# Kernel tuning notes

Measured on AMD Instinct MI355X. Metric: run time of the kernel, lower is better.

The kernel has to match this reference:

```python
import jax, jax.numpy as jnp
import numpy as np

B, S, D, H = 2, 2048, 1024, 16
HEAD_DIM = D // H  # 64


def setup_inputs() -> dict:
    key = jax.random.key(0)
    ks = jax.random.split(key, 7)
    x = jax.random.normal(ks[0], (B, S, D), dtype=jnp.float32)
    W_q = jax.random.normal(ks[1], (D, D), dtype=jnp.float32) * 0.02
    W_k = jax.random.normal(ks[2], (D, D), dtype=jnp.float32) * 0.02
    W_v = jax.random.normal(ks[3], (D, D), dtype=jnp.float32) * 0.02
    W_o = jax.random.normal(ks[4], (D, D), dtype=jnp.float32) * 0.02 / np.sqrt(2 * 12)
    b_o = jnp.zeros((D,), dtype=jnp.float32)
    # Ragged prefix attention_mask: per-row valid lengths in [S/2, S];
    # row 0 forced to full length so max_valid_len == S statically (jit-safe).
    lengths = jax.random.randint(ks[5], (B,), S // 2, S + 1)
    lengths = lengths.at[0].set(S)
    attention_mask = (jnp.arange(S)[None, :] < lengths[:, None]).astype(jnp.float32)
    return {"x": x, "attention_mask": attention_mask, "W_q": W_q, "W_k": W_k,
            "W_v": W_v, "W_o": W_o, "b_o": b_o}


def reference(x, attention_mask, W_q, W_k, W_v, W_o, b_o):
    b, s, d = x.shape
    h, hd = H, HEAD_DIM
    # QKV projections (no bias, qkv_bias=False)
    q = (x @ W_q.T).reshape(b, s, h, hd).transpose(0, 2, 1, 3)  # [b,h,s,hd]
    # Masking keys/values at invalid (padded) positions; for prefix masks this
    # is exactly the module's per-batch packing loop (max_valid_len == s).
    m = attention_mask[:, None, :, None]  # [b,1,s,1]
    k = ((x @ W_k.T).reshape(b, s, h, hd).transpose(0, 2, 1, 3)) * m
    v = ((x @ W_v.T).reshape(b, s, h, hd).transpose(0, 2, 1, 3)) * m
    # Naive causal attention, same op order as the torch module:
    # mask with -inf first, then scale by 1/sqrt(head_dim), then softmax.
    causal = jnp.triu(jnp.ones((s, s), dtype=bool), 1)  # True above diagonal
    scores = jnp.einsum('bhqd,bhkd->bhqk', q, k)
    scores = jnp.where(causal[None, None], -jnp.inf, scores)
    att = jax.nn.softmax(scores / jnp.sqrt(jnp.float32(hd)), axis=-1)
    ctx = jnp.einsum('bhqk,bhkd->bhqd', att, v)  # [b,h,s,hd]
    ctx = ctx.transpose(0, 2, 1, 3).reshape(b, s, d)
    # Output projection (dropout is inference no-op)
    return ctx @ W_o.T + b_o
```

## Files before the change

kernel.cpp:

```cpp
#include <hip/hip_runtime.h>

#define B_  2
#define S_  2048
#define D_  1024
#define H_  16
#define HD_ 64
#define N3_ 3072
#define M_  4096

typedef _Float16 f16;
typedef _Float16 f16x2 __attribute__((ext_vector_type(2)));
typedef _Float16 f16x4 __attribute__((ext_vector_type(4)));
typedef _Float16 f16x8 __attribute__((ext_vector_type(8)));
typedef float    f32x4 __attribute__((ext_vector_type(4)));

__device__ __forceinline__ void async16(const f16* g, f16* l) {
  __builtin_amdgcn_global_load_lds(
      (const __attribute__((address_space(1))) unsigned int*)g,
      (__attribute__((address_space(3))) unsigned int*)l, 16, 0, 0);
}

__device__ __forceinline__ f16x2 pkrtz(float a, float b) {
  return __builtin_bit_cast(f16x2, __builtin_amdgcn_cvt_pkrtz(a, b));
}

__device__ __forceinline__ float vexp2(float x) {
  float r; asm("v_exp_f32 %0, %1" : "=v"(r) : "v"(x)); return r;
}

__global__ __launch_bounds__(256)
void cvt_all(const float* __restrict__ x,
             const float* __restrict__ Wq, const float* __restrict__ Wk,
             const float* __restrict__ Wv, const float* __restrict__ Wo,
             f16* __restrict__ xb, f16* __restrict__ wdst, float qscale) {
  const int i = blockIdx.x * 256 + threadIdx.x;
  const int XN4 = M_ * D_ / 4;
  const int WN4 = D_ * D_ / 4;
  const float* src;
  f16* dst;
  float scale = 1.0f;
  int j;
  if (i < XN4) {
    src = x; dst = xb; j = i;
  } else {
    int k = i - XN4;
    int m = k >> 18;
    j = k & (WN4 - 1);
    src = (m == 0) ? Wq : (m == 1) ? Wk : (m == 2) ? Wv : Wo;
    if (m == 0) scale = qscale;
    dst = wdst + (size_t)m * D_ * D_;
  }
  float4 v = ((const float4*)src)[j];
  f16x4 o = { (f16)(v.x * scale), (f16)(v.y * scale),
              (f16)(v.z * scale), (f16)(v.w * scale) };
  ((f16x4*)dst)[j] = o;
}

__global__ __launch_bounds__(256)
void gemm_qkv(const f16* __restrict__ A, const f16* __restrict__ Bw,
              f16* __restrict__ Cq, f16* __restrict__ vtout,
              const float* __restrict__ mask) {
  __shared__ f16 As0[64 * 64];
  __shared__ f16 Bs0[128 * 64];
  __shared__ f16 As1[64 * 64];
  __shared__ f16 Bs1[128 * 64];

  const int tid  = threadIdx.x;
  const int lane = tid & 63;
  const int w    = tid >> 6;
  const int lcol = lane & 15;
  const int quad = lane >> 4;
  const int lx   = lcol & 7;
  const int wave_m = w >> 1, wave_n = w & 1;

  const int lin  = blockIdx.x;
  const int xcd  = lin & 7;
  const int c    = lin >> 3;
  const int mIdx = c / 12;
  const int nIdx = c - mIdx * 12;
  const int m0 = ((xcd >> 1) * 16 + mIdx) * 64;
  const int n0 = ((xcd & 1) * 12 + nIdx) * 128;

  const int rr  = lane >> 3;
  const int gch = (lane & 7) ^ rr;

  const f16* gA[2];
  const f16* gB[4];
#pragma unroll
  for (int i = 0; i < 2; i++) {
    int seg = 2 * w + i;
    gA[i] = A + (size_t)(m0 + seg * 8 + rr) * D_ + gch * 8;
  }
#pragma unroll
  for (int i = 0; i < 4; i++) {
    int seg = i * 4 + w;
    gB[i] = Bw + (size_t)(n0 + seg * 8 + rr) * D_ + gch * 8;
  }

  int offA[2], offB[4];
#pragma unroll
  for (int i = 0; i < 2; i++) offA[i] = (wave_m * 32 + i * 16 + lcol) * 64;
#pragma unroll
  for (int i = 0; i < 4; i++) offB[i] = (wave_n * 64 + i * 16 + lcol) * 64;

  const f32x4 zero = {0.f, 0.f, 0.f, 0.f};
  f32x4 acc[2][4];
#pragma unroll
  for (int i = 0; i < 2; i++)
#pragma unroll
    for (int j = 0; j < 4; j++) acc[i][j] = zero;

  auto stage = [&](int k0, f16* sA, f16* sB) {
#pragma unroll
    for (int i = 0; i < 2; i++) async16(gA[i] + k0, sA + (2 * w + i) * 512);
#pragma unroll
    for (int i = 0; i < 4; i++) async16(gB[i] + k0, sB + (i * 4 + w) * 512);
  };
  auto compute = [&](const f16* sA, const f16* sB) {
#pragma unroll
    for (int ks = 0; ks < 2; ks++) {
      const int co = ((quad + 4 * ks) ^ lx) * 8;
      f16x8 af[2], bf[4];
#pragma unroll
      for (int i = 0; i < 2; i++) af[i] = *(const f16x8*)(sA + offA[i] + co);
#pragma unroll
      for (int i = 0; i < 4; i++) bf[i] = *(const f16x8*)(sB + offB[i] + co);
#pragma unroll
      for (int mi = 0; mi < 2; mi++)
#pragma unroll
        for (int ni = 0; ni < 4; ni++)
          acc[mi][ni] = __builtin_amdgcn_mfma_f32_16x16x32_f16(
              af[mi], bf[ni], acc[mi][ni], 0, 0, 0);
    }
  };

  stage(0, As0, Bs0);
  for (int it = 0; it < 14; it += 2) {
    stage((it + 1) * 64, As1, Bs1);
    asm volatile("s_waitcnt vmcnt(6)\ns_barrier" ::: "memory");
    compute(As0, Bs0);
    asm volatile("s_barrier" ::: "memory");
    stage((it + 2) * 64, As0, Bs0);
    asm volatile("s_waitcnt vmcnt(6)\ns_barrier" ::: "memory");
    compute(As1, Bs1);
    asm volatile("s_barrier" ::: "memory");
  }
  stage(15 * 64, As1, Bs1);
  asm volatile("s_waitcnt vmcnt(6)\ns_barrier" ::: "memory");
  compute(As0, Bs0);
  asm volatile("s_waitcnt vmcnt(0)\ns_barrier" ::: "memory");
  compute(As1, Bs1);

#pragma unroll
  for (int mi = 0; mi < 2; mi++) {
    const int mgb = m0 + wave_m * 32 + mi * 16 + quad * 4;
    const int bb = mgb >> 11, s = mgb & (S_ - 1);
    const float mk0 = mask[mgb], mk1 = mask[mgb + 1];
    const float mk2 = mask[mgb + 2], mk3 = mask[mgb + 3];
    const float mks[4] = {mk0, mk1, mk2, mk3};
    if (n0 >= 2 * D_) {
#pragma unroll
      for (int ni = 0; ni < 4; ni++) {
        const int vcol = n0 - 2 * D_ + wave_n * 64 + ni * 16 + lcol;
        f16x4 v = { (f16)(acc[mi][ni][0] * mk0), (f16)(acc[mi][ni][1] * mk1),
                    (f16)(acc[mi][ni][2] * mk2), (f16)(acc[mi][ni][3] * mk3) };
        *(f16x4*)(vtout +
                  ((size_t)(bb * 16 + (vcol >> 6)) * 64 + (vcol & 63)) * S_ + s) = v;
      }
    } else {
      const bool kmask = (n0 >= D_);
#pragma unroll
      for (int r = 0; r < 4; r++) {
        const float mk = kmask ? mks[r] : 1.0f;
#pragma unroll
        for (int ni = 0; ni < 4; ni++) {
          int ng = n0 + wave_n * 64 + ni * 16 + lcol;
          Cq[(size_t)(mgb + r) * N3_ + ng] = (f16)(acc[mi][ni][r] * mk);
        }
      }
    }
  }
}

__global__ __launch_bounds__(256)
void gemm_proj(const f16* __restrict__ A, const f16* __restrict__ Bw,
               float* __restrict__ Cf, const float* __restrict__ bias) {
  __shared__ f16 As[64 * 64];
  __shared__ f16 Bs[128 * 64];

  const int tid  = threadIdx.x;
  const int lane = tid & 63;
  const int w    = tid >> 6;
  const int lcol = lane & 15;
  const int quad = lane >> 4;
  const int lx   = lcol & 7;
  const int wave_m = w >> 1, wave_n = w & 1;

  const int m0 = blockIdx.y * 64;
  const int n0 = blockIdx.x * 128;

  const int rr  = lane >> 3;
  const int gch = (lane & 7) ^ rr;

  const f16* gA[2];
  const f16* gB[4];
  f16* lA[2];
  f16* lB[4];
#pragma unroll
  for (int i = 0; i < 2; i++) {
    int seg = 2 * w + i;
    gA[i] = A + (size_t)(m0 + seg * 8 + rr) * D_ + gch * 8;
    lA[i] = As + seg * 512;
  }
#pragma unroll
  for (int i = 0; i < 4; i++) {
    int seg = i * 4 + w;
    gB[i] = Bw + (size_t)(n0 + seg * 8 + rr) * D_ + gch * 8;
    lB[i] = Bs + seg * 512;
  }

  int offA[2], offB[4];
#pragma unroll
  for (int i = 0; i < 2; i++) offA[i] = (wave_m * 32 + i * 16 + lcol) * 64;
#pragma unroll
  for (int i = 0; i < 4; i++) offB[i] = (wave_n * 64 + i * 16 + lcol) * 64;

  const f32x4 zero = {0.f, 0.f, 0.f, 0.f};
  f32x4 acc[2][4];
#pragma unroll
  for (int i = 0; i < 2; i++)
#pragma unroll
    for (int j = 0; j < 4; j++) acc[i][j] = zero;

  for (int k0 = 0; k0 < D_; k0 += 64) {
    __syncthreads();
#pragma unroll
    for (int i = 0; i < 2; i++) async16(gA[i] + k0, lA[i]);
#pragma unroll
    for (int i = 0; i < 4; i++) async16(gB[i] + k0, lB[i]);
    __syncthreads();

#pragma unroll
    for (int ks = 0; ks < 2; ks++) {
      const int co = ((quad + 4 * ks) ^ lx) * 8;
      f16x8 af[2], bf[4];
#pragma unroll
      for (int i = 0; i < 2; i++) af[i] = *(const f16x8*)(As + offA[i] + co);
#pragma unroll
      for (int i = 0; i < 4; i++) bf[i] = *(const f16x8*)(Bs + offB[i] + co);
#pragma unroll
      for (int mi = 0; mi < 2; mi++)
#pragma unroll
        for (int ni = 0; ni < 4; ni++)
          acc[mi][ni] = __builtin_amdgcn_mfma_f32_16x16x32_f16(
              af[mi], bf[ni], acc[mi][ni], 0, 0, 0);
    }
  }

#pragma unroll
  for (int mi = 0; mi < 2; mi++) {
#pragma unroll
    for (int r = 0; r < 4; r++) {
      int mg = m0 + wave_m * 32 + mi * 16 + quad * 4 + r;
#pragma unroll
      for (int ni = 0; ni < 4; ni++) {
        int ng = n0 + wave_n * 64 + ni * 16 + lcol;
        Cf[(size_t)mg * D_ + ng] = acc[mi][ni][r] + bias[ng];
      }
    }
  }
}

__global__ __launch_bounds__(128)
void flash_attn8(const f16* __restrict__ qkv, const f16* __restrict__ vt,
                 f16* __restrict__ ctx, float* __restrict__ part) {
  __shared__ f16 Ks[64 * 64];
  __shared__ f16 Vs[64 * 64];

  const int tid  = threadIdx.x;
  const int lane = tid & 63;
  const int w    = tid >> 6;
  const int lcol = lane & 15;
  const int quad = lane >> 4;
  const int lx   = lcol & 7;

  const int id   = blockIdx.x;
  const int bh   = (id & 7) + 8 * ((id >> 3) & 3);
  const int u    = id >> 5;
  const int p    = u & 15;
  const int role = u >> 4;
  const int g    = 31 - p;
  const int b    = bh >> 4, h = bh & 15;

  const int rsub = lane >> 3;
  const int gch  = (lane & 7) ^ rsub;
  const f16* Kg = qkv + (size_t)b * S_ * N3_ + D_ + h * HD_;
  const f16* Vg = vt + (size_t)bh * HD_ * S_;

  int srow[4];
  f16 *ldsK[4], *ldsV[4];
#pragma unroll
  for (int i = 0; i < 4; i++) {
    const int r0 = w * 32 + i * 8;
    srow[i] = r0 + rsub;
    ldsK[i] = Ks + r0 * 64;
    ldsV[i] = Vs + r0 * 64;
  }

  const f32x4 zero = {0.f, 0.f, 0.f, 0.f};
  f32x4 o0[4], o1[4];
  float lp0, lp1;

  auto run = [&](int qt, int ktb, int kte) {
    const int qrow0 = qt * 64 + w * 32 + lcol;
    const int qrow1 = qrow0 + 16;
    const f16* Qp0 = qkv + (size_t)(b * S_ + qrow0) * N3_ + h * HD_;
    const f16* Qp1 = qkv + (size_t)(b * S_ + qrow1) * N3_ + h * HD_;
    const f16x8 qa0 = *(const f16x8*)(Qp0 + quad * 8);
    const f16x8 qa1 = *(const f16x8*)(Qp0 + 32 + quad * 8);
    const f16x8 qb0 = *(const f16x8*)(Qp1 + quad * 8);
    const f16x8 qb1 = *(const f16x8*)(Qp1 + 32 + quad * 8);
#pragma unroll
    for (int i = 0; i < 4; i++) { o0[i] = zero; o1[i] = zero; }
    lp0 = 0.f; lp1 = 0.f;

    for (int kt = ktb; kt < kte; kt++) {
      const int kbase = kt * 64;
      __syncthreads();
#pragma unroll
      for (int i = 0; i < 4; i++)
        async16(Kg + (size_t)(kbase + srow[i]) * N3_ + gch * 8, ldsK[i]);
#pragma unroll
      for (int i = 0; i < 4; i++)
        async16(Vg + (size_t)srow[i] * S_ + kbase + gch * 8, ldsV[i]);
      __syncthreads();

      f32x4 sc0[4], sc1[4];
#pragma unroll
      for (int ct = 0; ct < 4; ct++) {
        const f16* kr = Ks + (ct * 16 + lcol) * 64;
        f16x8 kf0 = *(const f16x8*)(kr + ((quad    ) ^ lx) * 8);
        f16x8 kf1 = *(const f16x8*)(kr + ((quad + 4) ^ lx) * 8);
        f32x4 z0 = zero;
        z0 = __builtin_amdgcn_mfma_f32_16x16x32_f16(kf0, qa0, z0, 0, 0, 0);
        z0 = __builtin_amdgcn_mfma_f32_16x16x32_f16(kf1, qa1, z0, 0, 0, 0);
        sc0[ct] = z0;
        f32x4 z1 = zero;
        z1 = __builtin_amdgcn_mfma_f32_16x16x32_f16(kf0, qb0, z1, 0, 0, 0);
        z1 = __builtin_amdgcn_mfma_f32_16x16x32_f16(kf1, qb1, z1, 0, 0, 0);
        sc1[ct] = z1;
      }

      if (kt == qt) {
        const int qoff0 = w * 32 + lcol;
        const int qoff1 = qoff0 + 16;
#pragma unroll
        for (int ct = 0; ct < 4; ct++) {
          const int koff = ct * 16 + quad * 4;
#pragma unroll
          for (int r = 0; r < 4; r++) {
            if (koff + r > qoff0) sc0[ct][r] = -1e30f;
            if (koff + r > qoff1) sc1[ct][r] = -1e30f;
          }
        }
      }

      f16x4 pf0[4], pf1[4];
#pragma unroll
      for (int ct = 0; ct < 4; ct++) {
        float a0 = vexp2(sc0[ct][0]), a1 = vexp2(sc0[ct][1]);
        float a2 = vexp2(sc0[ct][2]), a3 = vexp2(sc0[ct][3]);
        lp0 += (a0 + a1) + (a2 + a3);
        f16x2 alo = pkrtz(a0, a1);
        f16x2 ahi = pkrtz(a2, a3);
        f16x4 pa = { alo[0], alo[1], ahi[0], ahi[1] };
        pf0[ct] = pa;
        float b0 = vexp2(sc1[ct][0]), b1 = vexp2(sc1[ct][1]);
        float b2 = vexp2(sc1[ct][2]), b3 = vexp2(sc1[ct][3]);
        lp1 += (b0 + b1) + (b2 + b3);
        f16x2 blo = pkrtz(b0, b1);
        f16x2 bhi = pkrtz(b2, b3);
        f16x4 pb = { blo[0], blo[1], bhi[0], bhi[1] };
        pf1[ct] = pb;
      }

#pragma unroll
      for (int ht = 0; ht < 4; ht++) {
        const f16* vr = Vs + (ht * 16 + lcol) * 64 + (quad & 1) * 4;
#pragma unroll
        for (int ct = 0; ct < 4; ct++) {
          f16x4 vf = *(const f16x4*)(vr + (((2 * ct + (quad >> 1)) ^ lx) * 8));
          o0[ht] = __builtin_amdgcn_mfma_f32_16x16x16f16(vf, pf0[ct], o0[ht], 0, 0, 0);
          o1[ht] = __builtin_amdgcn_mfma_f32_16x16x16f16(vf, pf1[ct], o1[ht], 0, 0, 0);
        }
      }
    }
    lp0 += __shfl_xor(lp0, 16);
    lp0 += __shfl_xor(lp0, 32);
    lp1 += __shfl_xor(lp1, 16);
    lp1 += __shfl_xor(lp1, 32);
  };

  const int row0 = w * 32 + lcol;
  const int row1 = row0 + 16;

  if (role == 0) {
    run(g, 0, 16);
    float* slot = part + ((size_t)(bh * 16 + p) * 2 + 0) * 4160;
#pragma unroll
    for (int ht = 0; ht < 4; ht++) {
      *(f32x4*)(slot + row0 * 64 + ht * 16 + quad * 4) = o0[ht];
      *(f32x4*)(slot + row1 * 64 + ht * 16 + quad * 4) = o1[ht];
    }
    if (quad == 0) {
      slot[4096 + row0] = lp0;
      slot[4096 + row1] = lp1;
    }
  } else {
    run(g, 16, g + 1);
    float* slot = part + ((size_t)(bh * 16 + p) * 2 + 1) * 4160;
#pragma unroll
    for (int ht = 0; ht < 4; ht++) {
      *(f32x4*)(slot + row0 * 64 + ht * 16 + quad * 4) = o0[ht];
      *(f32x4*)(slot + row1 * 64 + ht * 16 + quad * 4) = o1[ht];
    }
    if (quad == 0) {
      slot[4096 + row0] = lp0;
      slot[4096 + row1] = lp1;
    }

    run(p, 0, p + 1);
    const float inv0 = 1.f / lp0;
    const float inv1 = 1.f / lp1;
    f16* cp0 = ctx + (size_t)(b * S_ + p * 64 + row0) * D_ + h * HD_ + quad * 4;
    f16* cp1 = ctx + (size_t)(b * S_ + p * 64 + row1) * D_ + h * HD_ + quad * 4;
#pragma unroll
    for (int ht = 0; ht < 4; ht++) {
      f16x4 ov0 = { (f16)(o0[ht][0] * inv0), (f16)(o0[ht][1] * inv0),
                    (f16)(o0[ht][2] * inv0), (f16)(o0[ht][3] * inv0) };
      *(f16x4*)(cp0 + ht * 16) = ov0;
      f16x4 ov1 = { (f16)(o1[ht][0] * inv1), (f16)(o1[ht][1] * inv1),
                    (f16)(o1[ht][2] * inv1), (f16)(o1[ht][3] * inv1) };
      *(f16x4*)(cp1 + ht * 16) = ov1;
    }
  }
}

__global__ __launch_bounds__(256)
void attn_combine(const float* __restrict__ part, f16* __restrict__ ctx) {
  const int sid = blockIdx.x;
  const int bh  = sid >> 4, p = sid & 15;
  const int g   = 31 - p;
  const int b   = bh >> 4, h = bh & 15;
  const int t   = threadIdx.x;
  const int row = t >> 2;
  const int c0  = (t & 3) * 16;

  const float* sA = part + ((size_t)sid * 2 + 0) * 4160;
  const float* sB = part + ((size_t)sid * 2 + 1) * 4160;
  const float inv = 1.f / (sA[4096 + row] + sB[4096 + row]);
  const int qrow = g * 64 + row;
  f16* cp = ctx + (size_t)(b * S_ + qrow) * D_ + h * HD_ + c0;
#pragma unroll
  for (int j0 = 0; j0 < 16; j0 += 4) {
    f32x4 a  = *(const f32x4*)(sA + row * 64 + c0 + j0);
    f32x4 bb = *(const f32x4*)(sB + row * 64 + c0 + j0);
    f16x4 ov = { (f16)((a[0] + bb[0]) * inv), (f16)((a[1] + bb[1]) * inv),
                 (f16)((a[2] + bb[2]) * inv), (f16)((a[3] + bb[3]) * inv) };
    *(f16x4*)(cp + j0) = ov;
  }
}

extern "C" void kernel_launch(void* const* d_in, const int* in_sizes, int n_in,
                              void* d_out, int out_size, void* d_ws, size_t ws_size,
                              hipStream_t stream) {
  (void)in_sizes; (void)n_in; (void)out_size; (void)ws_size;
  const float* x  = (const float*)d_in[0];
  const float* am = (const float*)d_in[1];
  const float* Wq = (const float*)d_in[2];
  const float* Wk = (const float*)d_in[3];
  const float* Wv = (const float*)d_in[4];
  const float* Wo = (const float*)d_in[5];
  const float* bo = (const float*)d_in[6];
  float* out = (float*)d_out;

  f16* ws   = (f16*)d_ws;
  f16* wqkv = ws;
  f16* wo16 = wqkv + (size_t)3 * D_ * D_;
  f16* xb   = wo16 + (size_t)D_ * D_;
  f16* qkvb = xb + (size_t)M_ * D_;
  f16* vtb  = qkvb + (size_t)M_ * N3_;
  f16* ctxb = vtb + (size_t)M_ * D_;
  float* part = (float*)(ctxb + (size_t)M_ * D_);

  const float qscale = 0.125f * 1.4426950408889634f;

  cvt_all<<<dim3((M_ * D_ + 4 * D_ * D_) / 1024), 256, 0, stream>>>(
      x, Wq, Wk, Wv, Wo, xb, wqkv, qscale);

  gemm_qkv<<<dim3(1536), 256, 0, stream>>>(
      xb, wqkv, qkvb, vtb, am);
  flash_attn8<<<dim3(1024), 128, 0, stream>>>(qkvb, vtb, ctxb, part);
  attn_combine<<<dim3(512), 256, 0, stream>>>(part, ctxb);
  gemm_proj<<<dim3(D_ / 128, M_ / 64), 256, 0, stream>>>(
      ctxb, wo16, out, bo);
}
```

Baseline: 176.9 us.

## Double-buffer output projection GEMM and remap blocks for XCD locality

The output projection GEMM moves from a single LDS buffer with two barriers per k-step to a two-stage ping-pong pipeline. The next tile's async global-to-LDS load is issued before the current tile is computed, with explicit vmcnt waits and raw s_barriers. The grid also becomes 1D and is remapped so blocks on the same XCD share M/N tile neighborhoods, aiming to improve L2 reuse. This doubles LDS use per block, which may lower occupancy, and relies on hand-placed waitcnt values being correct.

```diff
diff --git a/kernel.cpp b/kernel.cpp
--- a/kernel.cpp
+++ b/kernel.cpp
@@ -185,8 +185,10 @@
 __global__ __launch_bounds__(256)
 void gemm_proj(const f16* __restrict__ A, const f16* __restrict__ Bw,
                float* __restrict__ Cf, const float* __restrict__ bias) {
-  __shared__ f16 As[64 * 64];
-  __shared__ f16 Bs[128 * 64];
+  __shared__ f16 As0[64 * 64];
+  __shared__ f16 Bs0[128 * 64];
+  __shared__ f16 As1[64 * 64];
+  __shared__ f16 Bs1[128 * 64];
 
   const int tid  = threadIdx.x;
   const int lane = tid & 63;
@@ -196,27 +198,28 @@
   const int lx   = lcol & 7;
   const int wave_m = w >> 1, wave_n = w & 1;
 
-  const int m0 = blockIdx.y * 64;
-  const int n0 = blockIdx.x * 128;
+  const int lin  = blockIdx.x;
+  const int xcd  = lin & 7;
+  const int c    = lin >> 3;
+  const int mIdx = c >> 2;
+  const int nIdx = c & 3;
+  const int m0 = ((xcd >> 1) * 16 + mIdx) * 64;
+  const int n0 = ((xcd & 1) * 4 + nIdx) * 128;
 
   const int rr  = lane >> 3;
   const int gch = (lane & 7) ^ rr;
 
   const f16* gA[2];
   const f16* gB[4];
-  f16* lA[2];
-  f16* lB[4];
 #pragma unroll
   for (int i = 0; i < 2; i++) {
     int seg = 2 * w + i;
     gA[i] = A + (size_t)(m0 + seg * 8 + rr) * D_ + gch * 8;
-    lA[i] = As + seg * 512;
   }
 #pragma unroll
   for (int i = 0; i < 4; i++) {
     int seg = i * 4 + w;
     gB[i] = Bw + (size_t)(n0 + seg * 8 + rr) * D_ + gch * 8;
-    lB[i] = Bs + seg * 512;
   }
 
   int offA[2], offB[4];
@@ -232,22 +235,21 @@
 #pragma unroll
     for (int j = 0; j < 4; j++) acc[i][j] = zero;
 
-  for (int k0 = 0; k0 < D_; k0 += 64) {
-    __syncthreads();
-#pragma unroll
-    for (int i = 0; i < 2; i++) async16(gA[i] + k0, lA[i]);
-#pragma unroll
-    for (int i = 0; i < 4; i++) async16(gB[i] + k0, lB[i]);
-    __syncthreads();
-
+  auto stage = [&](int k0, f16* sA, f16* sB) {
+#pragma unroll
+    for (int i = 0; i < 2; i++) async16(gA[i] + k0, sA + (2 * w + i) * 512);
+#pragma unroll
+    for (int i = 0; i < 4; i++) async16(gB[i] + k0, sB + (i * 4 + w) * 512);
+  };
+  auto compute = [&](const f16* sA, const f16* sB) {
 #pragma unroll
     for (int ks = 0; ks < 2; ks++) {
       const int co = ((quad + 4 * ks) ^ lx) * 8;
       f16x8 af[2], bf[4];
 #pragma unroll
-      for (int i = 0; i < 2; i++) af[i] = *(const f16x8*)(As + offA[i] + co);
-#pragma unroll
-      for (int i = 0; i < 4; i++) bf[i] = *(const f16x8*)(Bs + offB[i] + co);
+      for (int i = 0; i < 2; i++) af[i] = *(const f16x8*)(sA + offA[i] + co);
+#pragma unroll
+      for (int i = 0; i < 4; i++) bf[i] = *(const f16x8*)(sB + offB[i] + co);
 #pragma unroll
       for (int mi = 0; mi < 2; mi++)
 #pragma unroll
@@ -255,7 +257,24 @@
           acc[mi][ni] = __builtin_amdgcn_mfma_f32_16x16x32_f16(
               af[mi], bf[ni], acc[mi][ni], 0, 0, 0);
     }
-  }
+  };
+
+  stage(0, As0, Bs0);
+  for (int it = 0; it < 14; it += 2) {
+    stage((it + 1) * 64, As1, Bs1);
+    asm volatile("s_waitcnt vmcnt(6)\ns_barrier" ::: "memory");
+    compute(As0, Bs0);
+    asm volatile("s_barrier" ::: "memory");
+    stage((it + 2) * 64, As0, Bs0);
+    asm volatile("s_waitcnt vmcnt(6)\ns_barrier" ::: "memory");
+    compute(As1, Bs1);
+    asm volatile("s_barrier" ::: "memory");
+  }
+  stage(15 * 64, As1, Bs1);
+  asm volatile("s_waitcnt vmcnt(6)\ns_barrier" ::: "memory");
+  compute(As0, Bs0);
+  asm volatile("s_waitcnt vmcnt(0)\ns_barrier" ::: "memory");
+  compute(As1, Bs1);
 
 #pragma unroll
   for (int mi = 0; mi < 2; mi++) {
@@ -502,6 +521,6 @@
       xb, wqkv, qkvb, vtb, am);
   flash_attn8<<<dim3(1024), 128, 0, stream>>>(qkvb, vtb, ctxb, part);
   attn_combine<<<dim3(512), 256, 0, stream>>>(part, ctxb);
-  gemm_proj<<<dim3(D_ / 128, M_ / 64), 256, 0, stream>>>(
+  gemm_proj<<<dim3(512), 256, 0, stream>>>(
       ctxb, wo16, out, bo);
 }
```

Result: faster. 172.9 us (median of 4 runs) (-2.2%).
